# Kernel tuning notes

Hardware: AMD Instinct MI355X
Metric: run time of the kernel (lower is better)

The kernel has to match this reference:

```python
import jax, jax.numpy as jnp
import numpy as np

EPS = 1e-5

def _ln(x, g, b):
    mu = jnp.mean(x, axis=-1, keepdims=True)
    var = jnp.mean(jnp.square(x - mu), axis=-1, keepdims=True)
    return (x - mu) * jax.lax.rsqrt(var + EPS) * g + b

def setup_inputs() -> dict:
    key = jax.random.key(0)
    ks = jax.random.split(key, 12)
    B, N, CZ, CF, CP = 1, 512, 128, 384, 256
    s = 0.02
    return {
        'z': jax.random.normal(ks[0], (B, N, N, CZ), jnp.float32),
        'framepair_embed': jax.random.normal(ks[1], (B, N, N, CP), jnp.float32),
        'rigids_embed_flat': jax.random.normal(ks[2], (B, N, CF), jnp.float32),
        'rigids_to_res_idx': jax.random.randint(ks[3], (B, N), 0, N, dtype=jnp.int64),
        'rigids_mask': jnp.ones((B, N), jnp.float32),
        # nodepair_to_framepair_broadcast: LayerNorm(c_z) + Linear(c_z, c_framepair, bias=False)
        'ln_z_g': jnp.ones((CZ,), jnp.float32),
        'ln_z_b': jnp.zeros((CZ,), jnp.float32),
        'W_z': jax.random.normal(ks[4], (CZ, CP), jnp.float32) * s,
        # frame_ln + two bias-free broadcasts
        'ln_f_g': jnp.ones((CF,), jnp.float32),
        'ln_f_b': jnp.zeros((CF,), jnp.float32),
        'W_l': jax.random.normal(ks[5], (CF, CP), jnp.float32) * s,
        'W_m': jax.random.normal(ks[6], (CF, CP), jnp.float32) * s,
        # framepair_ffn: LN + Linear + ReLU + Linear + ReLU + Linear
        'ffn_ln_g': jnp.ones((CP,), jnp.float32),
        'ffn_ln_b': jnp.zeros((CP,), jnp.float32),
        'W1': jax.random.normal(ks[7], (CP, CP), jnp.float32) * s,
        'b1': jnp.zeros((CP,), jnp.float32),
        'W2': jax.random.normal(ks[8], (CP, CP), jnp.float32) * s,
        'b2': jnp.zeros((CP,), jnp.float32),
        'W3': jax.random.normal(ks[9], (CP, CP), jnp.float32) * s,
        'b3': jnp.zeros((CP,), jnp.float32),
    }

def reference(z, framepair_embed, rigids_embed_flat, rigids_to_res_idx, rigids_mask,
              ln_z_g, ln_z_b, W_z, ln_f_g, ln_f_b, W_l, W_m,
              ffn_ln_g, ffn_ln_b, W1, b1, W2, b2, W3, b3):
    # --- broadcast singles: row + column frame features into pair rep ---
    src = _ln(rigids_embed_flat, ln_f_g, ln_f_b)            # [B, N, CF]
    l = jnp.einsum('bnf,fp->bnp', src, W_l)                 # [B, N, CP]
    m = jnp.einsum('bnf,fp->bnp', src, W_m)
    fe = framepair_embed + l[:, :, None, :] + m[:, None, :, :]
    # --- broadcast pairs: irregular gather of residue-pair features ---
    ii = rigids_to_res_idx[0]                               # [N] (batch-0 indices, as in torch code)
    zb = z[:, ii[:, None], ii[None, :]]                     # [B, N, N, CZ]
    mk = rigids_mask[0]
    pair_mask = (mk[:, None] * mk[None, :])[None, :, :, None]
    zb = zb * pair_mask
    fe = fe + jnp.einsum('bijc,cp->bijp', _ln(zb, ln_z_g, ln_z_b), W_z)
    # --- framepair FFN with residual ---
    h = _ln(fe, ffn_ln_g, ffn_ln_b)
    h = jax.nn.relu(jnp.einsum('bijp,pq->bijq', h, W1) + b1)
    h = jax.nn.relu(jnp.einsum('bijp,pq->bijq', h, W2) + b2)
    fe = fe + jnp.einsum('bijp,pq->bijq', h, W3) + b3
    return fe
```

## Files before the change

### kernel.cpp

```cpp
#include <hip/hip_runtime.h>

#define NN 512
#define CZv 128
#define CFv 384
#define CPv 256
#define ROWS 64

typedef __attribute__((ext_vector_type(8))) short s16x8;
typedef __attribute__((ext_vector_type(4))) short s16x4;
typedef __attribute__((ext_vector_type(4))) float f32x4;

__device__ __forceinline__ unsigned short f2bf(float f) {
  unsigned int u = __builtin_bit_cast(unsigned int, f);
  u = (u + 0x7FFFu + ((u >> 16) & 1u)) >> 16;
  return (unsigned short)u;
}
__device__ __forceinline__ float bf2f(unsigned short h) {
  unsigned int u = ((unsigned int)h) << 16;
  return __builtin_bit_cast(float, u);
}
__device__ __forceinline__ unsigned int cvt_pk(float lo, float hi) {
  unsigned int r;
  asm("v_cvt_pk_bf16_f32 %0, %1, %2" : "=v"(r) : "v"(lo), "v"(hi));
  return r;
}
__device__ __forceinline__ s16x4 pack4(float a, float b, float c, float d) {
  unsigned int u0 = cvt_pk(a, b), u1 = cvt_pk(c, d);
  unsigned long long v = ((unsigned long long)u1 << 32) | u0;
  return __builtin_bit_cast(s16x4, v);
}

__global__ __launch_bounds__(256) void prep_kernel(
    const float* __restrict__ Wz, const float* __restrict__ W1,
    const float* __restrict__ W2, const float* __restrict__ W3,
    short* __restrict__ Wzf, short* __restrict__ W1f,
    short* __restrict__ W2f, short* __restrict__ W3f,
    const float* __restrict__ rf, const float* __restrict__ g, const float* __restrict__ b,
    const float* __restrict__ Wl, const float* __restrict__ Wm,
    float* __restrict__ lout, float* __restrict__ mout) {
  __shared__ float S[8][CFv];
  if (blockIdx.x < 896) {
    int o = blockIdx.x * 256 + threadIdx.x;
    const float* W;
    short* Wf;
    int lo;
    if (o < 32768) { W = Wz; Wf = Wzf; lo = o; }
    else if (o < 98304) { W = W1; Wf = W1f; lo = o - 32768; }
    else if (o < 163840) { W = W2; Wf = W2f; lo = o - 98304; }
    else { W = W3; Wf = W3f; lo = o - 163840; }
    int e = lo & 7;
    int l = (lo >> 3) & 63;
    int mt = (lo >> 9) & 15;
    int kk = lo >> 13;
    int k = kk * 32 + (l >> 4) * 8 + e;
    int p = mt * 16 + (l & 15);
    Wf[lo] = (short)f2bf(W[k * 256 + p]);
    return;
  }
  const int bb = blockIdx.x - 896;
  const int tid = threadIdx.x;
  const int w = tid >> 6;
  const int lane = tid & 63;
  for (int rr = 0; rr < 2; ++rr) {
    int r = bb * 8 + w * 2 + rr;
    const float* x = rf + (long)r * CFv;
    float v[6];
    float s1 = 0.f, s2 = 0.f;
#pragma unroll
    for (int q = 0; q < 6; ++q) {
      v[q] = x[lane + q * 64];
      s1 += v[q];
      s2 += v[q] * v[q];
    }
#pragma unroll
    for (int off = 1; off < 64; off <<= 1) {
      s1 += __shfl_xor(s1, off, 64);
      s2 += __shfl_xor(s2, off, 64);
    }
    float mu = s1 * (1.f / CFv);
    float va = s2 * (1.f / CFv) - mu * mu;
    float rs = rsqrtf(va + 1e-5f);
#pragma unroll
    for (int q = 0; q < 6; ++q) {
      int k = lane + q * 64;
      S[w * 2 + rr][k] = (v[q] - mu) * rs * g[k] + b[k];
    }
  }
  __syncthreads();
  float accl[8], accm[8];
#pragma unroll
  for (int r = 0; r < 8; ++r) { accl[r] = 0.f; accm[r] = 0.f; }
  for (int k = 0; k < CFv; ++k) {
    float wl = Wl[k * CPv + tid];
    float wm = Wm[k * CPv + tid];
#pragma unroll
    for (int r = 0; r < 8; ++r) {
      accl[r] += S[r][k] * wl;
      accm[r] += S[r][k] * wm;
    }
  }
#pragma unroll
  for (int r = 0; r < 8; ++r) {
    long rg = bb * 8 + r;
    lout[rg * CPv + tid] = accl[r];
    mout[rg * CPv + tid] = accm[r];
  }
}

__global__ __launch_bounds__(512, 4) void fused_main(
    const float* __restrict__ z, const float* __restrict__ fpe,
    const int* __restrict__ idx, const float* __restrict__ msk,
    const float* __restrict__ lnzg, const float* __restrict__ lnzb,
    const float* __restrict__ ffng, const float* __restrict__ ffnb,
    const float* __restrict__ b1p, const float* __restrict__ b2p, const float* __restrict__ b3p,
    const float* __restrict__ lws, const float* __restrict__ mws,
    const short* __restrict__ Wzf, const short* __restrict__ W1f,
    const short* __restrict__ W2f, const short* __restrict__ W3f,
    float* __restrict__ out) {
  __shared__ __align__(16) char X[ROWS * CPv * 2];
  __shared__ __align__(16) char Xres[ROWS * CPv * 2];
  __shared__ float SS[8][ROWS];
  __shared__ float SQ[8][ROWS];

  const int tid = threadIdx.x;
  const int w = tid >> 6;
  const int lane = tid & 63;
  const int l15 = lane & 15;
  const int lg = lane >> 4;
  const int mt0 = 2 * w;

  const int b = blockIdx.x;
  const int tile = (b & 7) * 512 + (b >> 3);
  const int i = tile >> 3;
  const int j0 = (tile & 7) * ROWS;
  const int r0 = tile * ROWS;

  f32x4 fe[4][2];
  {
    f32x4 lb[2];
    const float* lr = lws + (long)i * CPv;
#pragma unroll
    for (int mi = 0; mi < 2; ++mi)
      lb[mi] = *(const f32x4*)(lr + (mt0 + mi) * 16 + lg * 4);
#pragma unroll
    for (int nt = 0; nt < 4; ++nt) {
      const int row = nt * 16 + l15;
      const long rg = (long)r0 + row;
      const float* fpr = fpe + rg * CPv;
      const float* mr = mws + (long)(j0 + row) * CPv;
#pragma unroll
      for (int mi = 0; mi < 2; ++mi) {
        const int c0 = (mt0 + mi) * 16 + lg * 4;
        f32x4 a = *(const f32x4*)(fpr + c0);
        f32x4 mb = *(const f32x4*)(mr + c0);
        fe[nt][mi] = a + lb[mi] + mb;
      }
    }
  }

  {
    const int row = w * 8 + (lane & 7);
    const int seg = (lane >> 3) * 16;
    const int j = j0 + row;
    const int ia = idx[i];
    const int jb = idx[j];
    const float pm = msk[i] * msk[j];
    const float* zr = z + ((long)ia * NN + jb) * CZv + seg;
    f32x4 zv[4];
    float s1 = 0.f, s2 = 0.f;
#pragma unroll
    for (int q = 0; q < 4; ++q) {
      zv[q] = *(const f32x4*)(zr + q * 4);
#pragma unroll
      for (int e = 0; e < 4; ++e) {
        float v = zv[q][e] * pm;
        zv[q][e] = v;
        s1 += v;
        s2 += v * v;
      }
    }
    s1 += __shfl_xor(s1, 8, 64);
    s1 += __shfl_xor(s1, 16, 64);
    s1 += __shfl_xor(s1, 32, 64);
    s2 += __shfl_xor(s2, 8, 64);
    s2 += __shfl_xor(s2, 16, 64);
    s2 += __shfl_xor(s2, 32, 64);
    float mu = s1 * (1.f / CZv);
    float va = s2 * (1.f / CZv) - mu * mu;
    float rs = rsqrtf(va + 1e-5f);
    const int swz = (row & 7) << 4;
#pragma unroll
    for (int h = 0; h < 2; ++h) {
      const f32x4 g0 = *(const f32x4*)(lnzg + seg + h * 8);
      const f32x4 g1 = *(const f32x4*)(lnzg + seg + h * 8 + 4);
      const f32x4 q0 = *(const f32x4*)(lnzb + seg + h * 8);
      const f32x4 q1 = *(const f32x4*)(lnzb + seg + h * 8 + 4);
      float t[8];
#pragma unroll
      for (int e = 0; e < 4; ++e) {
        t[e] = (zv[h * 2][e] - mu) * rs * g0[e] + q0[e];
        t[4 + e] = (zv[h * 2 + 1][e] - mu) * rs * g1[e] + q1[e];
      }
      unsigned int u0 = cvt_pk(t[0], t[1]), u1 = cvt_pk(t[2], t[3]);
      unsigned int u2 = cvt_pk(t[4], t[5]), u3 = cvt_pk(t[6], t[7]);
      s16x8 hv;
      {
        unsigned int uu[4] = {u0, u1, u2, u3};
        hv = __builtin_bit_cast(s16x8, *(ulong2*)uu);
      }
      int off = (row * 256 + seg * 2 + h * 16) ^ swz;
      *(s16x8*)(X + off) = hv;
    }
  }
  __syncthreads();

  {
    const s16x8* Wp = (const s16x8*)Wzf;
    auto ldw = [&](int kk, s16x8(&a)[2]) {
      a[0] = Wp[(kk * 16 + mt0 + 0) * 64 + lane];
      a[1] = Wp[(kk * 16 + mt0 + 1) * 64 + lane];
    };
    auto step = [&](int kk, const s16x8(&a)[2]) {
#pragma unroll
      for (int nt = 0; nt < 4; ++nt) {
        const int row = nt * 16 + l15;
        int off = (row * 256 + kk * 64 + lg * 16) ^ ((row & 7) << 4);
        s16x8 bfr = *(const s16x8*)(X + off);
#pragma unroll
        for (int mi = 0; mi < 2; ++mi)
          fe[nt][mi] = __builtin_amdgcn_mfma_f32_16x16x32_bf16(a[mi], bfr, fe[nt][mi], 0, 0, 0);
      }
    };
    s16x8 afA[2], afB[2], afC[2];
    ldw(0, afA);
    ldw(1, afB);
    __builtin_amdgcn_s_setprio(1);
    ldw(2, afC);
    step(0, afA);
    ldw(3, afA);
    step(1, afB);
    step(2, afC);
    step(3, afA);
    __builtin_amdgcn_s_setprio(0);
  }

  float mu4[4], rs4[4];
  {
#pragma unroll
    for (int nt = 0; nt < 4; ++nt) {
      float s = 0.f, q = 0.f;
#pragma unroll
      for (int mi = 0; mi < 2; ++mi)
#pragma unroll
        for (int e = 0; e < 4; ++e) {
          float v = fe[nt][mi][e];
          s += v;
          q += v * v;
        }
      s += __shfl_xor(s, 16, 64);
      s += __shfl_xor(s, 32, 64);
      q += __shfl_xor(q, 16, 64);
      q += __shfl_xor(q, 32, 64);
      if (lane < 16) {
        SS[w][nt * 16 + lane] = s;
        SQ[w][nt * 16 + lane] = q;
      }
    }
    __syncthreads();
#pragma unroll
    for (int nt = 0; nt < 4; ++nt) {
      const int row = nt * 16 + l15;
      float ts = 0.f, tq = 0.f;
#pragma unroll
      for (int ww = 0; ww < 8; ++ww) {
        ts += SS[ww][row];
        tq += SQ[ww][row];
      }
      float mu = ts * (1.f / CPv);
      float va = tq * (1.f / CPv) - mu * mu;
      mu4[nt] = mu;
      rs4[nt] = rsqrtf(va + 1e-5f);
    }
  }

#pragma unroll
  for (int mi = 0; mi < 2; ++mi) {
    const int c0 = (mt0 + mi) * 16 + lg * 4;
    const f32x4 g4 = *(const f32x4*)(ffng + c0);
    const f32x4 b4 = *(const f32x4*)(ffnb + c0);
#pragma unroll
    for (int nt = 0; nt < 4; ++nt) {
      const int row = nt * 16 + l15;
      const int swz = (row & 7) << 4;
      float h0 = (fe[nt][mi][0] - mu4[nt]) * rs4[nt] * g4[0] + b4[0];
      float h1 = (fe[nt][mi][1] - mu4[nt]) * rs4[nt] * g4[1] + b4[1];
      float h2 = (fe[nt][mi][2] - mu4[nt]) * rs4[nt] * g4[2] + b4[2];
      float h3 = (fe[nt][mi][3] - mu4[nt]) * rs4[nt] * g4[3] + b4[3];
      s16x4 hv = pack4(h0, h1, h2, h3);
      s16x4 fv = pack4(fe[nt][mi][0], fe[nt][mi][1], fe[nt][mi][2], fe[nt][mi][3]);
      int off = (row * 512 + c0 * 2) ^ swz;
      *(s16x4*)(X + off) = hv;
      *(s16x4*)(Xres + off) = fv;
    }
  }
  __syncthreads();

  auto ffn_gemm = [&](const short* Wf, f32x4(&acc)[4][2]) {
    const s16x8* Wp = (const s16x8*)Wf;
    auto ldw = [&](int kk, s16x8(&a)[2]) {
      a[0] = Wp[(kk * 16 + mt0 + 0) * 64 + lane];
      a[1] = Wp[(kk * 16 + mt0 + 1) * 64 + lane];
    };
    auto step = [&](int kk, const s16x8(&a)[2]) {
#pragma unroll
      for (int nt = 0; nt < 4; ++nt) {
        const int row = nt * 16 + l15;
        int off = (row * 512 + kk * 64 + lg * 16) ^ ((row & 7) << 4);
        s16x8 bfr = *(const s16x8*)(X + off);
#pragma unroll
        for (int mi = 0; mi < 2; ++mi)
          acc[nt][mi] = __builtin_amdgcn_mfma_f32_16x16x32_bf16(a[mi], bfr, acc[nt][mi], 0, 0, 0);
      }
    };
    s16x8 afA[2], afB[2], afC[2];
    ldw(0, afA);
    ldw(1, afB);
    __builtin_amdgcn_s_setprio(1);
    ldw(2, afC);
    step(0, afA);
    ldw(3, afA);
    step(1, afB);
    ldw(4, afB);
    step(2, afC);
    ldw(5, afC);
    step(3, afA);
    ldw(6, afA);
    step(4, afB);
    ldw(7, afB);
    step(5, afC);
    step(6, afA);
    step(7, afB);
    __builtin_amdgcn_s_setprio(0);
  };

  auto write_relu = [&](f32x4(&acc)[4][2]) {
#pragma unroll
    for (int nt = 0; nt < 4; ++nt) {
      const int row = nt * 16 + l15;
      const int swz = (row & 7) << 4;
#pragma unroll
      for (int mi = 0; mi < 2; ++mi) {
        const int c0 = (mt0 + mi) * 16 + lg * 4;
        float v0 = fmaxf(acc[nt][mi][0], 0.f);
        float v1 = fmaxf(acc[nt][mi][1], 0.f);
        float v2 = fmaxf(acc[nt][mi][2], 0.f);
        float v3 = fmaxf(acc[nt][mi][3], 0.f);
        s16x4 hv = pack4(v0, v1, v2, v3);
        int off = (row * 512 + c0 * 2) ^ swz;
        *(s16x4*)(X + off) = hv;
      }
    }
  };

  f32x4 hacc[4][2];
#pragma unroll
  for (int mi = 0; mi < 2; ++mi) {
    const f32x4 bini = *(const f32x4*)(b1p + (mt0 + mi) * 16 + lg * 4);
#pragma unroll
    for (int nt = 0; nt < 4; ++nt) hacc[nt][mi] = bini;
  }
  ffn_gemm(W1f, hacc);
  __syncthreads();
  write_relu(hacc);
  __syncthreads();

#pragma unroll
  for (int mi = 0; mi < 2; ++mi) {
    const f32x4 bini = *(const f32x4*)(b2p + (mt0 + mi) * 16 + lg * 4);
#pragma unroll
    for (int nt = 0; nt < 4; ++nt) hacc[nt][mi] = bini;
  }
  ffn_gemm(W2f, hacc);
  __syncthreads();
  write_relu(hacc);
  __syncthreads();

#pragma unroll
  for (int mi = 0; mi < 2; ++mi) {
    const f32x4 b34 = *(const f32x4*)(b3p + (mt0 + mi) * 16 + lg * 4);
    const int c0 = (mt0 + mi) * 16 + lg * 4;
#pragma unroll
    for (int nt = 0; nt < 4; ++nt) {
      const int row = nt * 16 + l15;
      const int swz = (row & 7) << 4;
      int off = (row * 512 + c0 * 2) ^ swz;
      s16x4 fv = *(const s16x4*)(Xres + off);
#pragma unroll
      for (int e = 0; e < 4; ++e)
        hacc[nt][mi][e] = bf2f((unsigned short)fv[e]) + b34[e];
    }
  }
  ffn_gemm(W3f, hacc);
#pragma unroll
  for (int nt = 0; nt < 4; ++nt) {
    const long rg = (long)r0 + nt * 16 + l15;
#pragma unroll
    for (int mi = 0; mi < 2; ++mi) {
      const int c0 = (mt0 + mi) * 16 + lg * 4;
      *(f32x4*)(out + rg * CPv + c0) = hacc[nt][mi];
    }
  }
}

extern "C" void kernel_launch(void* const* d_in, const int* in_sizes, int n_in,
                              void* d_out, int out_size, void* d_ws, size_t ws_size,
                              hipStream_t stream) {
  const float* z = (const float*)d_in[0];
  const float* fpe = (const float*)d_in[1];
  const float* rf = (const float*)d_in[2];
  const int* idx = (const int*)d_in[3];
  const float* msk = (const float*)d_in[4];
  const float* lnzg = (const float*)d_in[5];
  const float* lnzb = (const float*)d_in[6];
  const float* Wz = (const float*)d_in[7];
  const float* lnfg = (const float*)d_in[8];
  const float* lnfb = (const float*)d_in[9];
  const float* Wl = (const float*)d_in[10];
  const float* Wm = (const float*)d_in[11];
  const float* ffng = (const float*)d_in[12];
  const float* ffnb = (const float*)d_in[13];
  const float* W1 = (const float*)d_in[14];
  const float* b1 = (const float*)d_in[15];
  const float* W2 = (const float*)d_in[16];
  const float* b2 = (const float*)d_in[17];
  const float* W3 = (const float*)d_in[18];
  const float* b3 = (const float*)d_in[19];
  float* out = (float*)d_out;

  char* ws = (char*)d_ws;
  float* lws = (float*)ws;
  float* mws = (float*)(ws + 512 * 1024);
  short* Wzf = (short*)(ws + 1024 * 1024);
  short* W1f = (short*)(ws + 1024 * 1024 + 64 * 1024);
  short* W2f = (short*)(ws + 1024 * 1024 + 192 * 1024);
  short* W3f = (short*)(ws + 1024 * 1024 + 320 * 1024);

  prep_kernel<<<960, 256, 0, stream>>>(Wz, W1, W2, W3, Wzf, W1f, W2f, W3f,
                                       rf, lnfg, lnfb, Wl, Wm, lws, mws);
  fused_main<<<4096, 512, 0, stream>>>(z, fpe, idx, msk, lnzg, lnzb, ffng, ffnb,
                                       b1, b2, b3, lws, mws, Wzf, W1f, W2f, W3f, out);
}
```

Measured before the change: 298.9 us.

## Keep residual in registers instead of LDS and double-buffer weight loads

Drops the Xres shared-memory buffer that held the bf16 residual. The fp32 fe accumulators now stay live in registers through the FFN and seed the final GEMM directly. This removes 32KB of LDS per block and the pack/unpack round trip, and it keeps the residual in full fp32 precision. The weight-fragment prefetch is also simplified from a three-buffer schedule to a two-buffer loop. In exchange, register pressure rises because fe stays live across three GEMMs, which could cause spills under the launch bound of 512 threads and 4 blocks.

Result: slower. 366.6 us (+22.6%).

```diff
diff --git a/kernel.cpp b/kernel.cpp
--- a/kernel.cpp
+++ b/kernel.cpp
@@ -14,10 +14,6 @@
   unsigned int u = __builtin_bit_cast(unsigned int, f);
   u = (u + 0x7FFFu + ((u >> 16) & 1u)) >> 16;
   return (unsigned short)u;
-}
-__device__ __forceinline__ float bf2f(unsigned short h) {
-  unsigned int u = ((unsigned int)h) << 16;
-  return __builtin_bit_cast(float, u);
 }
 __device__ __forceinline__ unsigned int cvt_pk(float lo, float hi) {
   unsigned int r;
@@ -118,7 +114,6 @@
     const short* __restrict__ W2f, const short* __restrict__ W3f,
     float* __restrict__ out) {
   __shared__ __align__(16) char X[ROWS * CPv * 2];
-  __shared__ __align__(16) char Xres[ROWS * CPv * 2];
   __shared__ float SS[8][ROWS];
   __shared__ float SQ[8][ROWS];
 
@@ -216,11 +211,18 @@
 
   {
     const s16x8* Wp = (const s16x8*)Wzf;
-    auto ldw = [&](int kk, s16x8(&a)[2]) {
-      a[0] = Wp[(kk * 16 + mt0 + 0) * 64 + lane];
-      a[1] = Wp[(kk * 16 + mt0 + 1) * 64 + lane];
-    };
-    auto step = [&](int kk, const s16x8(&a)[2]) {
+    s16x8 af[2][2];
+#pragma unroll
+    for (int mi = 0; mi < 2; ++mi) af[0][mi] = Wp[(mt0 + mi) * 64 + lane];
+    __builtin_amdgcn_s_setprio(1);
+#pragma unroll
+    for (int kk = 0; kk < 4; ++kk) {
+      const int cur = kk & 1;
+      if (kk < 3) {
+#pragma unroll
+        for (int mi = 0; mi < 2; ++mi)
+          af[cur ^ 1][mi] = Wp[((kk + 1) * 16 + mt0 + mi) * 64 + lane];
+      }
 #pragma unroll
       for (int nt = 0; nt < 4; ++nt) {
         const int row = nt * 16 + l15;
@@ -228,19 +230,9 @@
         s16x8 bfr = *(const s16x8*)(X + off);
 #pragma unroll
         for (int mi = 0; mi < 2; ++mi)
-          fe[nt][mi] = __builtin_amdgcn_mfma_f32_16x16x32_bf16(a[mi], bfr, fe[nt][mi], 0, 0, 0);
-      }
-    };
-    s16x8 afA[2], afB[2], afC[2];
-    ldw(0, afA);
-    ldw(1, afB);
-    __builtin_amdgcn_s_setprio(1);
-    ldw(2, afC);
-    step(0, afA);
-    ldw(3, afA);
-    step(1, afB);
-    step(2, afC);
-    step(3, afA);
+          fe[nt][mi] = __builtin_amdgcn_mfma_f32_16x16x32_bf16(af[cur][mi], bfr, fe[nt][mi], 0, 0, 0);
+      }
+    }
     __builtin_amdgcn_s_setprio(0);
   }
 
@@ -297,21 +289,26 @@
       float h2 = (fe[nt][mi][2] - mu4[nt]) * rs4[nt] * g4[2] + b4[2];
       float h3 = (fe[nt][mi][3] - mu4[nt]) * rs4[nt] * g4[3] + b4[3];
       s16x4 hv = pack4(h0, h1, h2, h3);
-      s16x4 fv = pack4(fe[nt][mi][0], fe[nt][mi][1], fe[nt][mi][2], fe[nt][mi][3]);
       int off = (row * 512 + c0 * 2) ^ swz;
       *(s16x4*)(X + off) = hv;
-      *(s16x4*)(Xres + off) = fv;
     }
   }
   __syncthreads();
 
   auto ffn_gemm = [&](const short* Wf, f32x4(&acc)[4][2]) {
     const s16x8* Wp = (const s16x8*)Wf;
-    auto ldw = [&](int kk, s16x8(&a)[2]) {
-      a[0] = Wp[(kk * 16 + mt0 + 0) * 64 + lane];
-      a[1] = Wp[(kk * 16 + mt0 + 1) * 64 + lane];
-    };
-    auto step = [&](int kk, const s16x8(&a)[2]) {
+    s16x8 af[2][2];
+#pragma unroll
+    for (int mi = 0; mi < 2; ++mi) af[0][mi] = Wp[(mt0 + mi) * 64 + lane];
+    __builtin_amdgcn_s_setprio(1);
+#pragma unroll
+    for (int kk = 0; kk < 8; ++kk) {
+      const int cur = kk & 1;
+      if (kk < 7) {
+#pragma unroll
+        for (int mi = 0; mi < 2; ++mi)
+          af[cur ^ 1][mi] = Wp[((kk + 1) * 16 + mt0 + mi) * 64 + lane];
+      }
 #pragma unroll
       for (int nt = 0; nt < 4; ++nt) {
         const int row = nt * 16 + l15;
@@ -319,27 +316,9 @@
         s16x8 bfr = *(const s16x8*)(X + off);
 #pragma unroll
         for (int mi = 0; mi < 2; ++mi)
-          acc[nt][mi] = __builtin_amdgcn_mfma_f32_16x16x32_bf16(a[mi], bfr, acc[nt][mi], 0, 0, 0);
-      }
-    };
-    s16x8 afA[2], afB[2], afC[2];
-    ldw(0, afA);
-    ldw(1, afB);
-    __builtin_amdgcn_s_setprio(1);
-    ldw(2, afC);
-    step(0, afA);
-    ldw(3, afA);
-    step(1, afB);
-    ldw(4, afB);
-    step(2, afC);
-    ldw(5, afC);
-    step(3, afA);
-    ldw(6, afA);
-    step(4, afB);
-    ldw(7, afB);
-    step(5, afC);
-    step(6, afA);
-    step(7, afB);
+          acc[nt][mi] = __builtin_amdgcn_mfma_f32_16x16x32_bf16(af[cur][mi], bfr, acc[nt][mi], 0, 0, 0);
+      }
+    }
     __builtin_amdgcn_s_setprio(0);
   };
 
@@ -388,26 +367,17 @@
 #pragma unroll
   for (int mi = 0; mi < 2; ++mi) {
     const f32x4 b34 = *(const f32x4*)(b3p + (mt0 + mi) * 16 + lg * 4);
-    const int c0 = (mt0 + mi) * 16 + lg * 4;
-#pragma unroll
-    for (int nt = 0; nt < 4; ++nt) {
-      const int row = nt * 16 + l15;
-      const int swz = (row & 7) << 4;
-      int off = (row * 512 + c0 * 2) ^ swz;
-      s16x4 fv = *(const s16x4*)(Xres + off);
-#pragma unroll
-      for (int e = 0; e < 4; ++e)
-        hacc[nt][mi][e] = bf2f((unsigned short)fv[e]) + b34[e];
-    }
-  }
-  ffn_gemm(W3f, hacc);
+#pragma unroll
+    for (int nt = 0; nt < 4; ++nt) fe[nt][mi] += b34;
+  }
+  ffn_gemm(W3f, fe);
 #pragma unroll
   for (int nt = 0; nt < 4; ++nt) {
     const long rg = (long)r0 + nt * 16 + l15;
 #pragma unroll
     for (int mi = 0; mi < 2; ++mi) {
       const int c0 = (mt0 + mi) * 16 + lg * 4;
-      *(f32x4*)(out + rg * CPv + c0) = hacc[nt][mi];
+      *(f32x4*)(out + rg * CPv + c0) = fe[nt][mi];
     }
   }
 }
```
